# Kernel optimization log

Hardware: AMD Instinct MI355X
Metric: run time of the kernel (lower is better)

## Reference

```python
import jax, jax.numpy as jnp
import numpy as np

B, L, E, H, V, DT, C = 64, 80, 256, 256, 30000, 100, 4
D = 4 * L * H  # BatchNorm / FC feature dim = max_length * hidden * 4
EPS = 1e-5


def setup_inputs() -> dict:
    key = jax.random.key(0)
    ks = jax.random.split(key, 20)
    n = lambda k, shape, s: jax.random.normal(k, shape, jnp.float32) * s
    g = 1.0 / np.sqrt(H)  # pytorch LSTM init scale
    return {
        "arg1": jax.random.randint(ks[0], (B, L), 0, V, dtype=jnp.int32),
        "arg2": jax.random.randint(ks[1], (B, L), 0, V, dtype=jnp.int32),
        "seq_lengths": jnp.full((B,), L, dtype=jnp.int32),
        "transE1": jax.random.normal(ks[2], (L, DT), jnp.float32),
        "transE2": jax.random.normal(ks[3], (L, DT), jnp.float32),
        # learned parameters
        "table": n(ks[4], (V, E), 0.05),                 # embedding (xavier-ish)
        "Wih_f": n(ks[5], (4 * H, E), g),
        "Whh_f": n(ks[6], (4 * H, H), g),
        "bih_f": n(ks[7], (4 * H,), g),
        "bhh_f": n(ks[8], (4 * H,), g),
        "Wih_b": n(ks[9], (4 * H, E), g),
        "Whh_b": n(ks[10], (4 * H, H), g),
        "bih_b": n(ks[11], (4 * H,), g),
        "bhh_b": n(ks[12], (4 * H,), g),
        "R": jax.random.uniform(ks[13], (2 * E, 2 * E), jnp.float32),  # torch.rand init
        "gamma": jnp.ones((D,), jnp.float32),
        "beta": jnp.zeros((D,), jnp.float32),
        "fcW": n(ks[14], (C, D), 0.01),
        "fcb": jnp.zeros((C,), jnp.float32),
    }


def _lstm_dir(x, Wih, Whh, b):
    # x: (B, L, E); pytorch gate order i, f, g, o
    xg = jnp.einsum('ble,ge->blg', x, Wih) + b          # (B, L, 4H)
    xg = jnp.swapaxes(xg, 0, 1)                         # (L, B, 4H)
    h0 = jnp.zeros((x.shape[0], Whh.shape[1]), x.dtype)

    def step(carry, g_t):
        h, c = carry
        gates = g_t + h @ Whh.T
        i, f, gg, o = jnp.split(gates, 4, axis=-1)
        c = jax.nn.sigmoid(f) * c + jax.nn.sigmoid(i) * jnp.tanh(gg)
        h = jax.nn.sigmoid(o) * jnp.tanh(c)
        return (h, c), h

    _, hs = jax.lax.scan(step, (h0, h0), xg)
    return jnp.swapaxes(hs, 0, 1)                       # (B, L, H)


def _bilstm(x, Wih_f, Whh_f, bih_f, bhh_f, Wih_b, Whh_b, bih_b, bhh_b):
    fwd = _lstm_dir(x, Wih_f, Whh_f, bih_f + bhh_f)
    bwd = _lstm_dir(x[:, ::-1], Wih_b, Whh_b, bih_b + bhh_b)[:, ::-1]
    return jnp.concatenate([fwd, bwd], axis=-1)         # (B, L, 2H)


def _forward(arg1, arg2, transE1, transE2, table, Wih_f, Whh_f, bih_f, bhh_f,
             Wih_b, Whh_b, bih_b, bhh_b, R, gamma, beta, fcW, fcb):
    # deal_transE: relation[i,j] = tanh(mean(arg1_word_i - arg2_word_j));
    # identical for every batch element -> block-diagonal kron.
    m1 = transE1.mean(axis=1)                           # (L,)
    m2 = transE2.mean(axis=1)                           # (L,)
    rel = jnp.tanh(m1[:, None] - m2[None, :])           # (L, L)
    kg = jax.lax.stop_gradient(jnp.kron(jnp.eye(B, dtype=rel.dtype), rel))  # (B*L, B*L)

    e1 = table[arg1]                                    # (B, L, E); dropout p=0 -> identity
    e2 = table[arg2]
    o1 = _bilstm(e1, Wih_f, Whh_f, bih_f, bhh_f, Wih_b, Whh_b, bih_b, bhh_b)
    o2 = _bilstm(e2, Wih_f, Whh_f, bih_f, bhh_f, Wih_b, Whh_b, bih_b, bhh_b)

    N = B * L
    t1 = o1.reshape(N, 2 * H)
    t2 = o2.reshape(N, 2 * H)

    last = jnp.tanh((t1 @ R) @ t2.T) + kg               # (N, N)
    sf1 = jax.nn.softmax(last, axis=1).mean(axis=0)[:, None]  # (N, 1)
    sf2 = jax.nn.softmax(last, axis=0).mean(axis=1)[:, None]  # (N, 1)

    out1 = (t1 * sf2).reshape(B, L, 2 * H)
    out2 = (t2 * sf1).reshape(B, L, 2 * H)
    out = jnp.concatenate([out1, out2], axis=1).reshape(B, -1)  # (B, D)

    # BatchNorm1d in training mode (biased variance over batch)
    mu = out.mean(axis=0)
    var = out.var(axis=0)
    xn = (out - mu) / jnp.sqrt(var + EPS) * gamma + beta

    logits = xn @ fcW.T + fcb
    return jax.nn.log_softmax(logits, axis=1)           # (B, C)


def reference(arg1, arg2, seq_lengths, transE1, transE2, table, Wih_f, Whh_f,
              bih_f, bhh_f, Wih_b, Whh_b, bih_b, bhh_b, R, gamma, beta, fcW, fcb):
    del seq_lengths  # only encodes (B, L), which are static here
    return _forward(arg1, arg2, transE1, transE2, table, Wih_f, Whh_f, bih_f,
                    bhh_f, Wih_b, Whh_b, bih_b, bhh_b, R, gamma, beta, fcW, fcb)
```

## Files before the change

### kernel.cpp

```cpp
#include <hip/hip_runtime.h>
#include <cstddef>
#include <cstdint>

typedef unsigned short ushort_t;

constexpr int B_ = 64, L_ = 80, E_ = 256, H_ = 256, C_ = 4, DT_ = 100;
constexpr int N_ = B_ * L_;
constexpr int G4_ = 4 * H_;
constexpr int DH2_ = 2 * H_;
constexpr int DF_ = 4 * L_ * H_;
constexpr float EPS_ = 1e-5f;
constexpr int FB_USH = 8192;

typedef short s8v __attribute__((ext_vector_type(8)));
typedef float f4v __attribute__((ext_vector_type(4)));
typedef ushort_t us8 __attribute__((ext_vector_type(8)));

__device__ inline ushort_t f2bf_rn(float x) {
    uint32_t u = __builtin_bit_cast(uint32_t, x);
    uint32_t r = (u + 0x7fffu + ((u >> 16) & 1u)) >> 16;
    return (ushort_t)r;
}
__device__ inline float bf2f(ushort_t h) {
    uint32_t u = ((uint32_t)h) << 16;
    return __builtin_bit_cast(float, u);
}
__device__ inline float rcpf(float x) { return __builtin_amdgcn_rcpf(x); }
__device__ inline float sigm(float x) { return rcpf(1.f + __expf(-x)); }
__device__ inline float tanh_fast(float x) {
    float e2 = __expf(2.f * x);
    return 1.f - 2.f * rcpf(1.f + e2);
}

#define MFMA_B16(a, b, c) __builtin_amdgcn_mfma_f32_16x16x32_bf16((a), (b), (c), 0, 0, 0)

__global__ void k_prep(const int* __restrict__ arg1, const int* __restrict__ arg2,
                       const float* __restrict__ table,
                       const float* __restrict__ tE1, const float* __restrict__ tE2,
                       const float* __restrict__ Wih_f, const float* __restrict__ Wih_b,
                       const float* __restrict__ bih_f, const float* __restrict__ bhh_f,
                       const float* __restrict__ bih_b, const float* __restrict__ bhh_b,
                       const float* __restrict__ R,
                       const float* __restrict__ Whh_f, const float* __restrict__ Whh_b,
                       ushort_t* __restrict__ ehi, ushort_t* __restrict__ elo,
                       ushort_t* __restrict__ Wchi, ushort_t* __restrict__ Wclo,
                       float* __restrict__ bcat,
                       ushort_t* __restrict__ Rthi, ushort_t* __restrict__ Rtlo,
                       ushort_t* __restrict__ Bhi, ushort_t* __restrict__ Blo,
                       ushort_t* __restrict__ fragbuf, int* __restrict__ flags,
                       float* __restrict__ rel) {
    __shared__ float m1[80], m2[80];
    int blk = blockIdx.x;
    int tid = threadIdx.x;
    if (blk < 10240) {
        int r = blk;
        int rr = (r >= N_) ? (r - N_) : r;
        int idx = (r >= N_) ? arg2[rr] : arg1[rr];
        float v = table[(size_t)idx * E_ + tid];
        ushort_t h = f2bf_rn(v);
        ehi[(size_t)r * E_ + tid] = h;
        elo[(size_t)r * E_ + tid] = f2bf_rn(v - bf2f(h));
    } else if (blk < 12288) {
        int i = (blk - 10240) * 256 + tid;
        if (i < 2 * G4_ * E_) {
            float v = (i < G4_ * E_) ? Wih_f[i] : Wih_b[i - G4_ * E_];
            ushort_t h = f2bf_rn(v);
            Wchi[i] = h;
            Wclo[i] = f2bf_rn(v - bf2f(h));
        }
        if (i < 2 * G4_)
            bcat[i] = (i < G4_) ? (bih_f[i] + bhh_f[i]) : (bih_b[i - G4_] + bhh_b[i - G4_]);
        if (i < 512 * 512) {
            int m = i >> 9, k = i & 511;
            float v = R[k * 512 + m];
            ushort_t h = f2bf_rn(v);
            Rthi[i] = h;
            Rtlo[i] = f2bf_rn(v - bf2f(h));
        }
    } else if (blk < 14336) {
        int idx = (blk - 12288) * 256 + tid;
        int e = idx & 7;
        int lane = (idx >> 3) & 63;
        int g = (idx >> 9) & 3;
        int kt = (idx >> 11) & 7;
        int w = (idx >> 14) & 15;
        int d = idx >> 18;
        int c = lane & 15, q = lane >> 4;
        int row = g * 256 + w * 16 + c;
        int k = kt * 32 + q * 8 + e;
        const float* W = d ? Whh_b : Whh_f;
        float v = W[row * 256 + k];
        ushort_t hi = f2bf_rn(v);
        Bhi[idx] = hi;
        Blo[idx] = f2bf_rn(v - bf2f(hi));
    } else if (blk < 14400) {
        int i = (blk - 14336) * 256 + tid;
        if (i < 256) flags[i] = 0;
        uint4* p = (uint4*)fragbuf;
        for (int jj = i; jj < 32768; jj += 64 * 256)
            p[jj] = make_uint4(0u, 0u, 0u, 0u);
    } else {
        if (tid < 80) {
            float s = 0.f;
            for (int k = 0; k < DT_; ++k) s += tE1[tid * DT_ + k];
            m1[tid] = s * (1.0f / DT_);
        } else if (tid < 160) {
            int i = tid - 80;
            float s = 0.f;
            for (int k = 0; k < DT_; ++k) s += tE2[i * DT_ + k];
            m2[i] = s * (1.0f / DT_);
        }
        __syncthreads();
        for (int idx = tid; idx < 80 * 80; idx += 256)
            rel[idx] = tanhf(m1[idx / 80] - m2[idx % 80]);
    }
}

__global__ __launch_bounds__(256, 2) void k_lstm9b(
        const float* __restrict__ xg,
        const ushort_t* __restrict__ Bhi, const ushort_t* __restrict__ Blo,
        ushort_t* __restrict__ o1hi, ushort_t* __restrict__ o1lo,
        ushort_t* __restrict__ o2hi, ushort_t* __restrict__ o2lo,
        ushort_t* __restrict__ fragbuf, int* __restrict__ flags) {
    const int bid = blockIdx.x;
    const int s = bid & 15;
    const int cg = (bid >> 4) & 7;
    const int d = bid >> 7;
    const int tid = threadIdx.x;
    const int g = tid >> 6, lane = tid & 63;
    const int c16 = lane & 15, qq = lane >> 4;

    __shared__ __align__(16) ushort_t Abuf[8192];
    __shared__ float pre[4][16][16];

    s8v bh[8], bl[8];
    {
        const s8v* BH = (const s8v*)Bhi;
        const s8v* BL = (const s8v*)Blo;
        int base = (d * 16 + s) * 2048 + g * 64 + lane;
        #pragma unroll
        for (int kt = 0; kt < 8; ++kt) {
            bh[kt] = BH[base + kt * 256];
            bl[kt] = BL[base + kt * 256];
        }
    }

    const int c_loc = tid >> 4, j = tid & 15;
    const int kglob = s * 16 + j;
    const int p_kt = kglob >> 5;
    const int p_q = (kglob & 31) >> 3, p_e = kglob & 7;
    const int p_lane = c_loc | (p_q << 4);
    const int fb_off = (p_kt * 64 + p_lane) * 8 + p_e;
    const int cc = cg * 16 + c_loc;
    const int w = cc >> 6, bb = cc & 63;
    ushort_t* ophi = w ? o2hi : o1hi;
    ushort_t* oplo = w ? o2lo : o1lo;
    float cst = 0.f;

    const int grp = bid >> 4;
    int* gflags = flags + grp * 16;
    const size_t fbbase = (size_t)grp * 2 * FB_USH;

    for (int t = 0; t < L_; ++t) {
        int l = d ? (L_ - 1 - t) : t;

        float xv[4];
        {
            const float* xp = xg + (size_t)(w * N_ + bb * L_ + l) * 2048
                              + d * 1024 + kglob;
            #pragma unroll
            for (int gg = 0; gg < 4; ++gg) xv[gg] = xp[gg * 256];
        }

        if (t > 0) {
            if (lane < 16) {
                while (__hip_atomic_load(&gflags[lane], __ATOMIC_RELAXED,
                                         __HIP_MEMORY_SCOPE_AGENT) < t)
                    __builtin_amdgcn_s_sleep(1);
            }
        }

        {
            const unsigned long long* src = (const unsigned long long*)(fragbuf
                + fbbase + (size_t)(t & 1) * FB_USH);
            unsigned long long* dst = (unsigned long long*)Abuf;
            #pragma unroll
            for (int r = 0; r < 8; ++r)
                dst[r * 256 + tid] = __hip_atomic_load(
                    &src[r * 256 + tid], __ATOMIC_RELAXED,
                    __HIP_MEMORY_SCOPE_AGENT);
        }
        __syncthreads();

        f4v acc = {0.f, 0.f, 0.f, 0.f};
        {
            const s8v* AH = (const s8v*)&Abuf[0];
            const s8v* AL = (const s8v*)&Abuf[4096];
            #pragma unroll
            for (int kt = 0; kt < 8; ++kt) {
                s8v ah = AH[kt * 64 + lane];
                s8v al = AL[kt * 64 + lane];
                acc = MFMA_B16(ah, bh[kt], acc);
                acc = MFMA_B16(ah, bl[kt], acc);
                acc = MFMA_B16(al, bh[kt], acc);
            }
        }
        #pragma unroll
        for (int r = 0; r < 4; ++r)
            pre[g][qq * 4 + r][c16] = acc[r];
        __syncthreads();

        ushort_t hh, hl;
        size_t oidx;
        {
            float pi = pre[0][c_loc][j] + xv[0];
            float pf = pre[1][c_loc][j] + xv[1];
            float pg = pre[2][c_loc][j] + xv[2];
            float po = pre[3][c_loc][j] + xv[3];
            float si = sigm(pi), sf_ = sigm(pf), so = sigm(po);
            cst = sf_ * cst + si * tanh_fast(pg);
            float h = so * tanh_fast(cst);
            oidx = (size_t)(bb * L_ + l) * DH2_ + d * H_ + kglob;
            hh = f2bf_rn(h);
            hl = f2bf_rn(h - bf2f(hh));
            ushort_t* fbn = fragbuf + fbbase + (size_t)((t + 1) & 1) * FB_USH;
            __hip_atomic_store(&fbn[fb_off], hh, __ATOMIC_RELAXED,
                               __HIP_MEMORY_SCOPE_AGENT);
            __hip_atomic_store(&fbn[4096 + fb_off], hl, __ATOMIC_RELAXED,
                               __HIP_MEMORY_SCOPE_AGENT);
        }
        __syncthreads();

        if (tid == 0)
            __hip_atomic_store(&flags[bid], t + 1, __ATOMIC_RELAXED,
                               __HIP_MEMORY_SCOPE_AGENT);

        ophi[oidx] = hh;
        oplo[oidx] = hl;
    }
}

__global__ __launch_bounds__(256) void k_gemm_bf(
        const ushort_t* __restrict__ Ahi, const ushort_t* __restrict__ Alo,
        const ushort_t* __restrict__ Bthi, const ushort_t* __restrict__ Btlo,
        const float* __restrict__ bias, float* __restrict__ Cout,
        ushort_t* __restrict__ Couthi, ushort_t* __restrict__ Coutlo,
        int M, int Nn, int K) {
    __shared__ ushort_t smpool[4][4096];
    const int tid = threadIdx.x;
    const int w = tid >> 6, lane = tid & 63;
    const int wr = w >> 1, wc = w & 1;
    const int c16 = lane & 15, q4 = lane >> 4;
    const int nbx = Nn >> 7;
    const int cpx = ((M >> 7) * nbx) >> 3;
    const int fid = blockIdx.x;
    const int swz = (fid & 7) * cpx + (fid >> 3);
    const int bx = swz % nbx, by = swz / nbx;
    const int r0 = by * 128, c0 = bx * 128;

    f4v acc[4][4] = {};
    const ushort_t* planes[4] = {
        Ahi + (size_t)r0 * K, Alo + (size_t)r0 * K,
        Bthi + (size_t)c0 * K, Btlo + (size_t)c0 * K };

    for (int kk = 0; kk < K; kk += 32) {
        #pragma unroll
        for (int p = 0; p < 4; ++p) {
            const ushort_t* src = planes[p] + kk;
            #pragma unroll
            for (int it = 0; it < 2; ++it) {
                int idx = it * 256 + tid;
                int row = idx >> 2, q = idx & 3;
                *(us8*)&smpool[p][(q * 128 + row) * 8] =
                    *(const us8*)&src[(size_t)row * K + q * 8];
            }
        }
        __syncthreads();
        s8v ah[4], al[4], bhv[4], blv[4];
        #pragma unroll
        for (int mi = 0; mi < 4; ++mi) {
            int ar = wr * 64 + mi * 16 + c16;
            ah[mi] = *(const s8v*)&smpool[0][(q4 * 128 + ar) * 8];
            al[mi] = *(const s8v*)&smpool[1][(q4 * 128 + ar) * 8];
        }
        #pragma unroll
        for (int ni = 0; ni < 4; ++ni) {
            int br = wc * 64 + ni * 16 + c16;
            bhv[ni] = *(const s8v*)&smpool[2][(q4 * 128 + br) * 8];
            blv[ni] = *(const s8v*)&smpool[3][(q4 * 128 + br) * 8];
        }
        #pragma unroll
        for (int mi = 0; mi < 4; ++mi)
            #pragma unroll
            for (int ni = 0; ni < 4; ++ni) {
                acc[mi][ni] = MFMA_B16(ah[mi], bhv[ni], acc[mi][ni]);
                acc[mi][ni] = MFMA_B16(ah[mi], blv[ni], acc[mi][ni]);
                acc[mi][ni] = MFMA_B16(al[mi], bhv[ni], acc[mi][ni]);
            }
        __syncthreads();
    }
    #pragma unroll
    for (int mi = 0; mi < 4; ++mi)
        #pragma unroll
        for (int rg = 0; rg < 4; ++rg) {
            int row = r0 + wr * 64 + mi * 16 + q4 * 4 + rg;
            #pragma unroll
            for (int ni = 0; ni < 4; ++ni) {
                int col = c0 + wc * 64 + ni * 16 + c16;
                float v = acc[mi][ni][rg] + (bias ? bias[col] : 0.f);
                size_t idx = (size_t)row * Nn + col;
                if (Couthi) {
                    ushort_t h = f2bf_rn(v);
                    Couthi[idx] = h;
                    Coutlo[idx] = f2bf_rn(v - bf2f(h));
                } else {
                    Cout[idx] = v;
                }
            }
        }
}

__global__ __launch_bounds__(256) void k_bigm(
        const ushort_t* __restrict__ uhi, const ushort_t* __restrict__ ulo,
        const ushort_t* __restrict__ vhi, const ushort_t* __restrict__ vlo,
        const float* __restrict__ rel, ushort_t* __restrict__ Ebf,
        float* __restrict__ rowpart, float* __restrict__ colpart) {
    __shared__ ushort_t smpool[4][4096];
    const int tid = threadIdx.x;
    const int w = tid >> 6, lane = tid & 63;
    const int wr = w >> 1, wc = w & 1;
    const int c16 = lane & 15, q4 = lane >> 4;
    const int fid = blockIdx.x;
    const int swz = (fid & 7) * 200 + (fid >> 3);
    const int bx = swz % 40, by = swz / 40;
    const int r0 = by * 128, c0 = bx * 128;

    f4v acc[4][4] = {};
    const ushort_t* planes[4] = {
        uhi + (size_t)r0 * DH2_, ulo + (size_t)r0 * DH2_,
        vhi + (size_t)c0 * DH2_, vlo + (size_t)c0 * DH2_ };

    for (int kk = 0; kk < 16; ++kk) {
        #pragma unroll
        for (int p = 0; p < 4; ++p) {
            const ushort_t* src = planes[p] + kk * 32;
            #pragma unroll
            for (int it = 0; it < 2; ++it) {
                int idx = it * 256 + tid;
                int row = idx >> 2, q = idx & 3;
                *(us8*)&smpool[p][(q * 128 + row) * 8] =
                    *(const us8*)&src[(size_t)row * DH2_ + q * 8];
            }
        }
        __syncthreads();
        s8v ah[4], al[4], bhv[4], blv[4];
        #pragma unroll
        for (int mi = 0; mi < 4; ++mi) {
            int ar = wr * 64 + mi * 16 + c16;
            ah[mi] = *(const s8v*)&smpool[0][(q4 * 128 + ar) * 8];
            al[mi] = *(const s8v*)&smpool[1][(q4 * 128 + ar) * 8];
        }
        #pragma unroll
        for (int ni = 0; ni < 4; ++ni) {
            int br = wc * 64 + ni * 16 + c16;
            bhv[ni] = *(const s8v*)&smpool[2][(q4 * 128 + br) * 8];
            blv[ni] = *(const s8v*)&smpool[3][(q4 * 128 + br) * 8];
        }
        #pragma unroll
        for (int mi = 0; mi < 4; ++mi)
            #pragma unroll
            for (int ni = 0; ni < 4; ++ni) {
                acc[mi][ni] = MFMA_B16(ah[mi], bhv[ni], acc[mi][ni]);
                acc[mi][ni] = MFMA_B16(ah[mi], blv[ni], acc[mi][ni]);
                acc[mi][ni] = MFMA_B16(al[mi], bhv[ni], acc[mi][ni]);
            }
        __syncthreads();
    }

    float* rowred = (float*)&smpool[0][0];
    float* colred = rowred + 128 * 32;

    int gcolv[4], bjv[4], ljv[4];
    #pragma unroll
    for (int ni = 0; ni < 4; ++ni) {
        int coll = wc * 64 + ni * 16 + c16;
        gcolv[ni] = c0 + coll;
        bjv[ni] = gcolv[ni] / 80;
        ljv[ni] = gcolv[ni] - bjv[ni] * 80;
    }
    float csumv[4] = {0.f, 0.f, 0.f, 0.f};
    #pragma unroll
    for (int mi = 0; mi < 4; ++mi) {
        #pragma unroll
        for (int rg = 0; rg < 4; ++rg) {
            int rowl = wr * 64 + mi * 16 + q4 * 4 + rg;
            int grow = r0 + rowl;
            int bi = grow / 80, li = grow - bi * 80;
            float rsum = 0.f;
            #pragma unroll
            for (int ni = 0; ni < 4; ++ni) {
                float v = tanhf(acc[mi][ni][rg]);
                if (bi == bjv[ni]) v += rel[li * 80 + ljv[ni]];
                ushort_t eb = f2bf_rn(__expf(v));
                Ebf[(size_t)grow * N_ + gcolv[ni]] = eb;
                float er = bf2f(eb);
                rsum += er;
                csumv[ni] += er;
            }
            rowred[rowl * 32 + wc * 16 + c16] = rsum;
        }
    }
    #pragma unroll
    for (int ni = 0; ni < 4; ++ni) {
        int coll = wc * 64 + ni * 16 + c16;
        colred[coll * 8 + wr * 4 + q4] = csumv[ni];
    }
    __syncthreads();
    if (tid < 128) {
        float ssum = 0.f;
        #pragma unroll
        for (int t = 0; t < 32; ++t) ssum += rowred[tid * 32 + t];
        rowpart[(size_t)bx * N_ + r0 + tid] = ssum;
    } else {
        int c = tid - 128;
        float ssum = 0.f;
        #pragma unroll
        for (int t = 0; t < 8; ++t) ssum += colred[c * 8 + t];
        colpart[(size_t)by * N_ + c0 + c] = ssum;
    }
}

__global__ void k_redsum(const float* __restrict__ rowpart, const float* __restrict__ colpart,
                         float* __restrict__ rowinv, float* __restrict__ colinv) {
    int i = blockIdx.x * blockDim.x + threadIdx.x;
    if (i < N_) {
        float rs = 0.f, cs = 0.f;
        for (int t = 0; t < 40; ++t) {
            rs += rowpart[(size_t)t * N_ + i];
            cs += colpart[(size_t)t * N_ + i];
        }
        rowinv[i] = 1.f / rs;
        colinv[i] = 1.f / cs;
    }
}

__global__ __launch_bounds__(256) void k_sfpass(
        const ushort_t* __restrict__ Ebf,
        const float* __restrict__ rowinv, const float* __restrict__ colinv,
        float* __restrict__ sf1part, float* __restrict__ sf2part) {
    const int tid = threadIdx.x;
    const int lane = tid & 63, wv = tid >> 6;
    const int col = blockIdx.x * 256 + tid;
    const int rc = blockIdx.y;
    const int r0 = rc * 320;
    __shared__ float rowp4[320][4];

    float cinv = colinv[col];
    float accC = 0.f;
    #pragma unroll 4
    for (int ii = 0; ii < 320; ++ii) {
        int row = r0 + ii;
        float e = bf2f(Ebf[(size_t)row * N_ + col]);
        accC += e * rowinv[row];
        float t2 = e * cinv;
        #pragma unroll
        for (int off = 32; off > 0; off >>= 1) t2 += __shfl_down(t2, off, 64);
        if (lane == 0) rowp4[ii][wv] = t2;
    }
    sf1part[(size_t)rc * N_ + col] = accC;
    __syncthreads();
    if (tid < 320) {
        float s = rowp4[tid][0] + rowp4[tid][1] + rowp4[tid][2] + rowp4[tid][3];
        sf2part[(size_t)blockIdx.x * N_ + r0 + tid] = s;
    }
}

__global__ void k_sfred(const float* __restrict__ sf1part,
                        const float* __restrict__ sf2part,
                        float* __restrict__ sf1, float* __restrict__ sf2) {
    int j = blockIdx.x * blockDim.x + threadIdx.x;
    if (j < N_) {
        float s1 = 0.f;
        for (int t = 0; t < 16; ++t) s1 += sf1part[(size_t)t * N_ + j];
        sf1[j] = s1 * (1.f / N_);
        float s2 = 0.f;
        for (int t = 0; t < 20; ++t) s2 += sf2part[(size_t)t * N_ + j];
        sf2[j] = s2 * (1.f / N_);
    }
}

__global__ void k_bnstats(const ushort_t* __restrict__ o1hi, const ushort_t* __restrict__ o1lo,
                          const ushort_t* __restrict__ o2hi, const ushort_t* __restrict__ o2lo,
                          const float* __restrict__ sf1, const float* __restrict__ sf2,
                          float* __restrict__ bnmu, float* __restrict__ bnrstd) {
    int f = blockIdx.x * 256 + threadIdx.x;
    int seg = f / (L_ * DH2_);
    int rem = f - seg * (L_ * DH2_);
    int l = rem >> 9, hh = rem & 511;
    const ushort_t* phi = seg ? o2hi : o1hi;
    const ushort_t* plo = seg ? o2lo : o1lo;
    const float* sf = seg ? sf1 : sf2;
    float s = 0.f, s2 = 0.f;
    for (int b = 0; b < B_; ++b) {
        int row = b * L_ + l;
        size_t idx = (size_t)row * DH2_ + hh;
        float x = (bf2f(phi[idx]) + bf2f(plo[idx])) * sf[row];
        s += x;
        s2 += x * x;
    }
    float mu = s * (1.f / B_);
    float v = fmaxf(s2 * (1.f / B_) - mu * mu, 0.f);
    bnmu[f] = mu;
    bnrstd[f] = rsqrtf(v + EPS_);
}

__global__ __launch_bounds__(256) void k_logits1(
        const ushort_t* __restrict__ o1hi, const ushort_t* __restrict__ o1lo,
        const ushort_t* __restrict__ o2hi, const ushort_t* __restrict__ o2lo,
        const float* __restrict__ sf1, const float* __restrict__ sf2,
        const float* __restrict__ bnmu, const float* __restrict__ bnrstd,
        const float* __restrict__ gamma, const float* __restrict__ beta,
        const float* __restrict__ fcW, float* __restrict__ part) {
    int b = blockIdx.x, ch = blockIdx.y;
    int tid = threadIdx.x;
    int f0 = ch * (DF_ / 5);
    float acc[4] = {0.f, 0.f, 0.f, 0.f};
    for (int f = f0 + tid; f < f0 + DF_ / 5; f += 256) {
        int seg = f / (L_ * DH2_);
        int rem = f - seg * (L_ * DH2_);
        int l = rem >> 9, hh = rem & 511;
        int row = b * L_ + l;
        size_t idx = (size_t)row * DH2_ + hh;
        const ushort_t* phi = seg ? o2hi : o1hi;
        const ushort_t* plo = seg ? o2lo : o1lo;
        float val = (bf2f(phi[idx]) + bf2f(plo[idx])) * (seg ? sf1 : sf2)[row];
        float xn = (val - bnmu[f]) * bnrstd[f] * gamma[f] + beta[f];
        #pragma unroll
        for (int c = 0; c < 4; ++c) acc[c] += xn * fcW[(size_t)c * DF_ + f];
    }
    __shared__ float red[4][257];
    #pragma unroll
    for (int c = 0; c < 4; ++c) red[c][tid] = acc[c];
    __syncthreads();
    for (int ss = 128; ss > 0; ss >>= 1) {
        if (tid < ss)
            #pragma unroll
            for (int c = 0; c < 4; ++c) red[c][tid] += red[c][tid + ss];
        __syncthreads();
    }
    if (tid < 4) part[((size_t)b * 5 + ch) * 4 + tid] = red[tid][0];
}

__global__ void k_logits2(const float* __restrict__ part,
                          const float* __restrict__ fcb,
                          float* __restrict__ dout) {
    int b = blockIdx.x;
    if (threadIdx.x == 0) {
        float lg[4], mx = -1e30f;
        #pragma unroll
        for (int c = 0; c < 4; ++c) {
            float v = fcb[c];
            for (int ch = 0; ch < 5; ++ch) v += part[((size_t)b * 5 + ch) * 4 + c];
            lg[c] = v;
            mx = fmaxf(mx, v);
        }
        float se = 0.f;
        #pragma unroll
        for (int c = 0; c < 4; ++c) se += expf(lg[c] - mx);
        float lse = mx + logf(se);
        #pragma unroll
        for (int c = 0; c < 4; ++c) dout[b * 4 + c] = lg[c] - lse;
    }
}

extern "C" void kernel_launch(void* const* d_in, const int* in_sizes, int n_in,
                              void* d_out, int out_size, void* d_ws, size_t ws_size,
                              hipStream_t stream) {
    const int* arg1 = (const int*)d_in[0];
    const int* arg2 = (const int*)d_in[1];
    const float* tE1 = (const float*)d_in[3];
    const float* tE2 = (const float*)d_in[4];
    const float* table = (const float*)d_in[5];
    const float* Wih_f = (const float*)d_in[6];
    const float* Whh_f = (const float*)d_in[7];
    const float* bih_f = (const float*)d_in[8];
    const float* bhh_f = (const float*)d_in[9];
    const float* Wih_b = (const float*)d_in[10];
    const float* Whh_b = (const float*)d_in[11];
    const float* bih_b = (const float*)d_in[12];
    const float* bhh_b = (const float*)d_in[13];
    const float* R = (const float*)d_in[14];
    const float* gamma = (const float*)d_in[15];
    const float* beta = (const float*)d_in[16];
    const float* fcW = (const float*)d_in[17];
    const float* fcb = (const float*)d_in[18];
    float* dout = (float*)d_out;

    float* ws = (float*)d_ws;
    size_t off = 0;
    auto alloc = [&](size_t n) { float* p = ws + off; off += n; return p; };

    constexpr size_t PL = (size_t)N_ * DH2_;

    float* rel = alloc(80 * 80);
    float* eplanes = alloc((size_t)2 * N_ * E_);
    float* Wcplanes = alloc((size_t)2 * G4_ * E_);
    float* bcat = alloc(2 * G4_);
    float* Rtplanes = alloc((size_t)262144);
    float* planesA = alloc(PL);
    float* planesU = alloc(PL);
    float* rowpart = alloc((size_t)40 * N_);
    float* colpart = alloc((size_t)40 * N_);
    float* rowinv = alloc(N_);
    float* colinv = alloc(N_);
    float* sf1part = alloc((size_t)16 * N_);
    float* sf2part = alloc((size_t)20 * N_);
    float* sf1 = alloc(N_);
    float* sf2 = alloc(N_);
    float* bnmu = alloc(DF_);
    float* bnrstd = alloc(DF_);
    float* lgpart = alloc((size_t)B_ * 5 * 4);
    ushort_t* Bhi = (ushort_t*)alloc(262144);
    ushort_t* Blo = (ushort_t*)alloc(262144);
    ushort_t* fragbuf = (ushort_t*)alloc(131072);
    int* flags = (int*)alloc(256);
    float* xg = alloc((size_t)N_ * N_);
    ushort_t* Ebf = (ushort_t*)xg;

    ushort_t* ehi = (ushort_t*)eplanes;
    ushort_t* elo = ehi + (size_t)2 * N_ * E_;
    ushort_t* Wchi = (ushort_t*)Wcplanes;
    ushort_t* Wclo = Wchi + (size_t)2 * G4_ * E_;
    ushort_t* Rthi = (ushort_t*)Rtplanes;
    ushort_t* Rtlo = Rthi + 512 * 512;
    ushort_t* o1hi = (ushort_t*)planesA;
    ushort_t* o1lo = o1hi + PL;
    ushort_t* uhi = (ushort_t*)planesU;
    ushort_t* ulo = uhi + PL;
    ushort_t* o2hi = ehi;
    ushort_t* o2lo = elo;

    k_prep<<<14401, 256, 0, stream>>>(arg1, arg2, table, tE1, tE2,
                                      Wih_f, Wih_b, bih_f, bhh_f, bih_b, bhh_b,
                                      R, Whh_f, Whh_b,
                                      ehi, elo, Wchi, Wclo, bcat, Rthi, Rtlo,
                                      Bhi, Blo, fragbuf, flags, rel);
    k_gemm_bf<<<1280, 256, 0, stream>>>(
        ehi, elo, Wchi, Wclo, bcat, xg, nullptr, nullptr, 2 * N_, 2048, E_);
    k_lstm9b<<<256, 256, 0, stream>>>(xg, Bhi, Blo,
                                      o1hi, o1lo, o2hi, o2lo, fragbuf, flags);
    k_gemm_bf<<<160, 256, 0, stream>>>(
        o1hi, o1lo, Rthi, Rtlo, nullptr, nullptr, uhi, ulo, N_, 512, 512);
    k_bigm<<<1600, 256, 0, stream>>>(
        uhi, ulo, o2hi, o2lo, rel, Ebf, rowpart, colpart);
    k_redsum<<<(N_ + 255) / 256, 256, 0, stream>>>(rowpart, colpart, rowinv, colinv);
    k_sfpass<<<dim3(20, 16), 256, 0, stream>>>(Ebf, rowinv, colinv, sf1part, sf2part);
    k_sfred<<<(N_ + 255) / 256, 256, 0, stream>>>(sf1part, sf2part, sf1, sf2);
    k_bnstats<<<DF_ / 256, 256, 0, stream>>>(o1hi, o1lo, o2hi, o2lo, sf1, sf2,
                                             bnmu, bnrstd);
    k_logits1<<<dim3(B_, 5), 256, 0, stream>>>(o1hi, o1lo, o2hi, o2lo, sf1, sf2,
                                               bnmu, bnrstd, gamma, beta, fcW, lgpart);
    k_logits2<<<B_, 64, 0, stream>>>(lgpart, fcb, dout);
}
```

Before: 744.1 us.

## Split softmax-mean pass into row and column kernels, tweak LSTM flag wait

The fused pass, which did a wave shuffle reduction per row for every element, is replaced by two kernels. A per-row kernel reduces each row of E against colinv to produce sf2 directly, and a column kernel reads packed bf16 pairs to accumulate sf1 partials. This drops the per-element shuffle reductions and the sf2 partial buffer, but reads the E matrix twice. Separately, the LSTM spin-wait now polls with the first 16 threads, sleeps longer between polls, and adds a block barrier after the wait.

After: 624.6 us. 1.19x faster.

```diff
diff --git a/kernel.cpp b/kernel.cpp
--- a/kernel.cpp
+++ b/kernel.cpp
@@ -25,6 +25,8 @@
     uint32_t u = ((uint32_t)h) << 16;
     return __builtin_bit_cast(float, u);
 }
+__device__ inline float bf2f_lo(uint32_t u) { return __builtin_bit_cast(float, u << 16); }
+__device__ inline float bf2f_hi(uint32_t u) { return __builtin_bit_cast(float, u & 0xffff0000u); }
 __device__ inline float rcpf(float x) { return __builtin_amdgcn_rcpf(x); }
 __device__ inline float sigm(float x) { return rcpf(1.f + __expf(-x)); }
 __device__ inline float tanh_fast(float x) {
@@ -116,7 +118,7 @@
     }
 }
 
-__global__ __launch_bounds__(256, 2) void k_lstm9b(
+__global__ __launch_bounds__(256, 2) void k_lstm9c(
         const float* __restrict__ xg,
         const ushort_t* __restrict__ Bhi, const ushort_t* __restrict__ Blo,
         ushort_t* __restrict__ o1hi, ushort_t* __restrict__ o1lo,
@@ -173,11 +175,12 @@
         }
 
         if (t > 0) {
-            if (lane < 16) {
-                while (__hip_atomic_load(&gflags[lane], __ATOMIC_RELAXED,
+            if (tid < 16) {
+                while (__hip_atomic_load(&gflags[tid], __ATOMIC_RELAXED,
                                          __HIP_MEMORY_SCOPE_AGENT) < t)
-                    __builtin_amdgcn_s_sleep(1);
-            }
+                    __builtin_amdgcn_s_sleep(2);
+            }
+            __syncthreads();
         }
 
         {
@@ -444,48 +447,52 @@
     }
 }
 
-__global__ __launch_bounds__(256) void k_sfpass(
-        const ushort_t* __restrict__ Ebf,
-        const float* __restrict__ rowinv, const float* __restrict__ colinv,
-        float* __restrict__ sf1part, float* __restrict__ sf2part) {
-    const int tid = threadIdx.x;
-    const int lane = tid & 63, wv = tid >> 6;
-    const int col = blockIdx.x * 256 + tid;
-    const int rc = blockIdx.y;
-    const int r0 = rc * 320;
-    __shared__ float rowp4[320][4];
-
-    float cinv = colinv[col];
-    float accC = 0.f;
+__global__ __launch_bounds__(256) void k_sf2b(const ushort_t* __restrict__ Ebf,
+                                              const float* __restrict__ colinv,
+                                              float* __restrict__ sf2) {
+    int i = blockIdx.x;
+    const uint32_t* Erow = (const uint32_t*)(Ebf + (size_t)i * N_);
+    float p = 0.f;
+    #pragma unroll 2
+    for (int j2 = threadIdx.x; j2 < N_ / 2; j2 += 256) {
+        uint32_t u = Erow[j2];
+        p += bf2f_lo(u) * colinv[j2 * 2] + bf2f_hi(u) * colinv[j2 * 2 + 1];
+    }
+    __shared__ float red[256];
+    red[threadIdx.x] = p;
+    __syncthreads();
+    for (int ss = 128; ss > 0; ss >>= 1) {
+        if (threadIdx.x < ss) red[threadIdx.x] += red[threadIdx.x + ss];
+        __syncthreads();
+    }
+    if (threadIdx.x == 0) sf2[i] = red[0] * (1.f / N_);
+}
+
+__global__ __launch_bounds__(256) void k_sf1b(const ushort_t* __restrict__ Ebf,
+                                              const float* __restrict__ rowinv,
+                                              float* __restrict__ sf1part) {
+    int cp = blockIdx.x * 256 + threadIdx.x;
+    int rc = blockIdx.y;
+    int r0 = rc * 320;
+    float a0 = 0.f, a1 = 0.f;
     #pragma unroll 4
     for (int ii = 0; ii < 320; ++ii) {
         int row = r0 + ii;
-        float e = bf2f(Ebf[(size_t)row * N_ + col]);
-        accC += e * rowinv[row];
-        float t2 = e * cinv;
-        #pragma unroll
-        for (int off = 32; off > 0; off >>= 1) t2 += __shfl_down(t2, off, 64);
-        if (lane == 0) rowp4[ii][wv] = t2;
-    }
-    sf1part[(size_t)rc * N_ + col] = accC;
-    __syncthreads();
-    if (tid < 320) {
-        float s = rowp4[tid][0] + rowp4[tid][1] + rowp4[tid][2] + rowp4[tid][3];
-        sf2part[(size_t)blockIdx.x * N_ + r0 + tid] = s;
-    }
-}
-
-__global__ void k_sfred(const float* __restrict__ sf1part,
-                        const float* __restrict__ sf2part,
-                        float* __restrict__ sf1, float* __restrict__ sf2) {
-    int j = blockIdx.x * blockDim.x + threadIdx.x;
-    if (j < N_) {
-        float s1 = 0.f;
-        for (int t = 0; t < 16; ++t) s1 += sf1part[(size_t)t * N_ + j];
-        sf1[j] = s1 * (1.f / N_);
-        float s2 = 0.f;
-        for (int t = 0; t < 20; ++t) s2 += sf2part[(size_t)t * N_ + j];
-        sf2[j] = s2 * (1.f / N_);
+        uint32_t u = *(const uint32_t*)(Ebf + (size_t)row * N_ + cp * 2);
+        float rinv = rowinv[row];
+        a0 += bf2f_lo(u) * rinv;
+        a1 += bf2f_hi(u) * rinv;
+    }
+    sf1part[(size_t)rc * N_ + cp * 2] = a0;
+    sf1part[(size_t)rc * N_ + cp * 2 + 1] = a1;
+}
+
+__global__ void k_sf1red(const float* __restrict__ sf1part, float* __restrict__ sf1) {
+    int jj = blockIdx.x * blockDim.x + threadIdx.x;
+    if (jj < N_) {
+        float s = 0.f;
+        for (int t = 0; t < 16; ++t) s += sf1part[(size_t)t * N_ + jj];
+        sf1[jj] = s * (1.f / N_);
     }
 }
 
@@ -614,7 +621,6 @@
     float* rowinv = alloc(N_);
     float* colinv = alloc(N_);
     float* sf1part = alloc((size_t)16 * N_);
-    float* sf2part = alloc((size_t)20 * N_);
     float* sf1 = alloc(N_);
     float* sf2 = alloc(N_);
     float* bnmu = alloc(DF_);
@@ -647,15 +653,16 @@
                                       Bhi, Blo, fragbuf, flags, rel);
     k_gemm_bf<<<1280, 256, 0, stream>>>(
         ehi, elo, Wchi, Wclo, bcat, xg, nullptr, nullptr, 2 * N_, 2048, E_);
-    k_lstm9b<<<256, 256, 0, stream>>>(xg, Bhi, Blo,
+    k_lstm9c<<<256, 256, 0, stream>>>(xg, Bhi, Blo,
                                       o1hi, o1lo, o2hi, o2lo, fragbuf, flags);
     k_gemm_bf<<<160, 256, 0, stream>>>(
         o1hi, o1lo, Rthi, Rtlo, nullptr, nullptr, uhi, ulo, N_, 512, 512);
     k_bigm<<<1600, 256, 0, stream>>>(
         uhi, ulo, o2hi, o2lo, rel, Ebf, rowpart, colpart);
     k_redsum<<<(N_ + 255) / 256, 256, 0, stream>>>(rowpart, colpart, rowinv, colinv);
-    k_sfpass<<<dim3(20, 16), 256, 0, stream>>>(Ebf, rowinv, colinv, sf1part, sf2part);
-    k_sfred<<<(N_ + 255) / 256, 256, 0, stream>>>(sf1part, sf2part, sf1, sf2);
+    k_sf2b<<<N_, 256, 0, stream>>>(Ebf, colinv, sf2);
+    k_sf1b<<<dim3(10, 16), 256, 0, stream>>>(Ebf, rowinv, sf1part);
+    k_sf1red<<<(N_ + 255) / 256, 256, 0, stream>>>(sf1part, sf1);
     k_bnstats<<<DF_ / 256, 256, 0, stream>>>(o1hi, o1lo, o2hi, o2lo, sf1, sf2,
                                              bnmu, bnrstd);
     k_logits1<<<dim3(B_, 5), 256, 0, stream>>>(o1hi, o1lo, o2hi, o2lo, sf1, sf2,
```
